# Kernel optimization log

Measured on AMD Instinct MI355X. Metric: run time of the kernel, lower is better.

The kernel has to match this reference:

```python
import jax, jax.numpy as jnp
from jax import lax
import numpy as np

TEMPERATURE = 0.8
TOP_P = 0.9
NEG_INF = -jnp.inf


def setup_inputs() -> dict:
    key = jax.random.key(0)
    k1, k2 = jax.random.split(key)
    B, V = 128, 128000
    logits = jax.random.normal(k1, (B, V), dtype=jnp.float32) * 4.0
    u = jax.random.uniform(k2, (B, 1), dtype=jnp.float32)  # replaces torch.rand in sample_multinomial
    return {"logits": logits, "u": u, "top_k": 50}


def _filtered_probs(logits, top_k):
    # temperature scaling
    x = logits / TEMPERATURE
    # ---- top-k filter: keep only the k largest per row (mask rest to -inf) ----
    kth = lax.top_k(x, top_k)[0][..., -1:]            # [B, 1] k-th largest value
    x = jnp.where(x < kth, NEG_INF, x)
    # ---- top-p (nucleus) filter ----
    sort_idx = jnp.argsort(-x, axis=-1)               # descending order, [B, V]
    sorted_x = jnp.take_along_axis(x, sort_idx, axis=-1)
    probs_sorted = jax.nn.softmax(sorted_x, axis=-1)  # -inf entries -> 0
    cdf = jnp.cumsum(probs_sorted, axis=-1)
    # remove tokens where cdf (shifted right by one, first kept) exceeds p
    remove_sorted = jnp.concatenate(
        [jnp.zeros_like(cdf[..., :1], dtype=bool), (cdf > TOP_P)[..., :-1]], axis=-1
    )
    inv = jnp.argsort(sort_idx, axis=-1)              # inverse permutation
    remove = jnp.take_along_axis(remove_sorted, inv, axis=-1)
    x = jnp.where(remove, NEG_INF, x)
    # final probabilities
    return jax.nn.softmax(x.astype(jnp.float32), axis=-1)


def reference(logits, u, top_k):
    probs = _filtered_probs(logits, top_k)            # [B, V]
    # inverse-CDF multinomial sample (matches sample_multinomial)
    csum = jnp.cumsum(probs, axis=-1)
    next_ids = jnp.sum(csum <= u, axis=-1, keepdims=True).astype(jnp.int32)  # [B, 1]
    return next_ids
```

## Files before the change

kernel.cpp:

```cpp
#include <hip/hip_runtime.h>
#include <math.h>


#define SLICES   16
#define SEGCAP   64
#define MSORT    1024

__device__ __forceinline__ unsigned fkey(float y) {
    unsigned b = __float_as_uint(y);
    return (b & 0x80000000u) ? ~b : (b | 0x80000000u);
}

__device__ __forceinline__ float block_sum(float v, int tid, float* wpart) {
#pragma unroll
    for (int off = 32; off > 0; off >>= 1) v += __shfl_down(v, off, 64);
    if ((tid & 63) == 0) wpart[tid >> 6] = v;
    __syncthreads();
    if (tid < 64) {
        float s = (tid < 16) ? wpart[tid] : 0.0f;
#pragma unroll
        for (int off = 8; off > 0; off >>= 1) s += __shfl_down(s, off, 64);
        if (tid == 0) wpart[0] = s;
    }
    __syncthreads();
    float s = wpart[0];
    __syncthreads();
    return s;
}

__device__ __forceinline__ void incl_scan(float* arr, int n, int tid, float* wpart) {
    float v = (tid < n) ? arr[tid] : 0.0f;
#pragma unroll
    for (int off = 1; off < 64; off <<= 1) {
        float o = __shfl_up(v, off, 64);
        if ((tid & 63) >= off) v += o;
    }
    if ((tid & 63) == 63) wpart[tid >> 6] = v;
    __syncthreads();
    if (tid < 64) {
        float w = (tid < 16) ? wpart[tid] : 0.0f;
#pragma unroll
        for (int off = 1; off < 16; off <<= 1) {
            float o = __shfl_up(w, off, 64);
            if (tid >= off) w += o;
        }
        if (tid < 16) wpart[tid] = w;
    }
    __syncthreads();
    const int wv = tid >> 6;
    const float base = (wv > 0) ? wpart[wv - 1] : 0.0f;
    if (tid < n) arr[tid] = v + base;
    __syncthreads();
}

__global__ __launch_bounds__(256)
void scan_kernel(const float* __restrict__ logits, int V,
                 int* __restrict__ scnt,
                 float* __restrict__ cy, int* __restrict__ ci)
{
    constexpr float YTH = 11.2f;
    __shared__ float lcy[SEGCAP];
    __shared__ int   lci[SEGCAP];
    __shared__ int   lcnt;

    const int tid = threadIdx.x;
    const int row = blockIdx.x / SLICES;
    const int sl  = blockIdx.x % SLICES;
    if (tid == 0) lcnt = 0;
    __syncthreads();

    const float* rowp = logits + (size_t)row * (size_t)V;
    const float4* rp4 = (const float4*)rowp;
    const int n4   = V >> 2;
    const int base = sl * 256 + tid;

#define PUSH4(vv, i4)                                                            \
    {                                                                            \
        float _m = fmaxf(fmaxf((vv).x, (vv).y), fmaxf((vv).z, (vv).w));          \
        if (_m >= YTH) {                                                         \
            if ((vv).x >= YTH) { int _p = atomicAdd(&lcnt, 1);                   \
                if (_p < SEGCAP) { lcy[_p] = (vv).x; lci[_p] = (i4) * 4;     } } \
            if ((vv).y >= YTH) { int _p = atomicAdd(&lcnt, 1);                   \
                if (_p < SEGCAP) { lcy[_p] = (vv).y; lci[_p] = (i4) * 4 + 1; } } \
            if ((vv).z >= YTH) { int _p = atomicAdd(&lcnt, 1);                   \
                if (_p < SEGCAP) { lcy[_p] = (vv).z; lci[_p] = (i4) * 4 + 2; } } \
            if ((vv).w >= YTH) { int _p = atomicAdd(&lcnt, 1);                   \
                if (_p < SEGCAP) { lcy[_p] = (vv).w; lci[_p] = (i4) * 4 + 3; } } \
        }                                                                        \
    }

    if (sl * 256 + 255 + 7 * 4096 < n4) {
        float4 a0 = rp4[base];
        float4 a1 = rp4[base + 4096];
        float4 a2 = rp4[base + 8192];
        float4 a3 = rp4[base + 12288];
        float4 a4 = rp4[base + 16384];
        float4 a5 = rp4[base + 20480];
        float4 a6 = rp4[base + 24576];
        float4 a7 = rp4[base + 28672];
        PUSH4(a0, base);
        PUSH4(a1, base + 4096);
        PUSH4(a2, base + 8192);
        PUSH4(a3, base + 12288);
        PUSH4(a4, base + 16384);
        PUSH4(a5, base + 20480);
        PUSH4(a6, base + 24576);
        PUSH4(a7, base + 28672);
    } else {
        const int nc = n4 - 1;
        int i0 = base,          c0 = min(i0, nc);
        int i1 = base + 4096,   c1 = min(i1, nc);
        int i2 = base + 8192,   c2 = min(i2, nc);
        int i3 = base + 12288,  c3 = min(i3, nc);
        int i4_ = base + 16384, c4 = min(i4_, nc);
        int i5 = base + 20480,  c5 = min(i5, nc);
        int i6 = base + 24576,  c6 = min(i6, nc);
        int i7 = base + 28672,  c7 = min(i7, nc);
        float4 a0 = rp4[c0];
        float4 a1 = rp4[c1];
        float4 a2 = rp4[c2];
        float4 a3 = rp4[c3];
        float4 a4 = rp4[c4];
        float4 a5 = rp4[c5];
        float4 a6 = rp4[c6];
        float4 a7 = rp4[c7];
        if (i0 < n4) PUSH4(a0, i0);
        if (i1 < n4) PUSH4(a1, i1);
        if (i2 < n4) PUSH4(a2, i2);
        if (i3 < n4) PUSH4(a3, i3);
        if (i4_ < n4) PUSH4(a4, i4_);
        if (i5 < n4) PUSH4(a5, i5);
        if (i6 < n4) PUSH4(a6, i6);
        if (i7 < n4) PUSH4(a7, i7);
    }
    for (int i = SLICES * 256 * 8 + sl * 256 + tid; i < n4; i += SLICES * 256) {
        float4 a = rp4[i];
        PUSH4(a, i);
    }
    if (sl == SLICES - 1) {
        for (int i = (n4 << 2) + tid; i < V; i += 256) {
            float y = rowp[i];
            if (y >= YTH) {
                int p = atomicAdd(&lcnt, 1);
                if (p < SEGCAP) { lcy[p] = y; lci[p] = i; }
            }
        }
    }
#undef PUSH4
    __syncthreads();

    const int cnt = lcnt;
    float* cyr = cy + ((size_t)row * SLICES + sl) * SEGCAP;
    int*   cir = ci + ((size_t)row * SLICES + sl) * SEGCAP;
    for (int p = tid; p < min(cnt, SEGCAP); p += 256) {
        cyr[p] = lcy[p];
        cir[p] = lci[p];
    }
    if (tid == 0) scnt[row * SLICES + sl] = cnt;
}

__global__ __launch_bounds__(1024)
void select_kernel(const float* __restrict__ logits,
                   const float* __restrict__ uvec,
                   const int* __restrict__ topk_p,
                   const int* __restrict__ scnt,
                   const float* __restrict__ cy, const int* __restrict__ ci,
                   int* __restrict__ out, int V)
{
    constexpr float TEMP = 0.8f;
    constexpr float TOPP = 0.9f;
    constexpr float XTH2 = 16.0f;

    __shared__ float gv[MSORT];
    __shared__ int   gi[MSORT];
    __shared__ float cv[MSORT];
    __shared__ int   cidx[MSORT];
    __shared__ float sq[MSORT];
    __shared__ float wpart[16];
    __shared__ float kth_sh;
    __shared__ int   segoff[SLICES + 1];
    __shared__ int   bad_sh, hi_cnt, cpos, scount, cnt_sh, M_sh, tie_cnt, L_cnt, ans_sh;

    const int tid  = threadIdx.x;
    const int lane = tid & 63;
    const int row  = blockIdx.x;
    const int nth  = blockDim.x;
    const int k_in = *topk_p;

    const float* rowp = logits + (size_t)row * (size_t)V;

    if (tid == 0) { hi_cnt = 0; cpos = 0; scount = 0;
                    tie_cnt = 0; L_cnt = 0; ans_sh = V; }
    if (tid < 64) {
        int c = (tid < SLICES) ? scnt[row * SLICES + tid] : 0;
        int bad = (tid < SLICES) && (c > SEGCAP);
        int acc = min(c, SEGCAP);
#pragma unroll
        for (int off = 1; off < SLICES; off <<= 1) {
            int o = __shfl_up(acc, off, 64);
            if (tid >= off) acc += o;
        }
        if (tid < SLICES) segoff[tid + 1] = acc;
        if (tid == 0) segoff[0] = 0;
        unsigned long long bm = __ballot(bad);
        if (tid == 0) bad_sh = (bm != 0ULL);
    }
    __syncthreads();

    const int M_all = segoff[SLICES];
    int M;
    if (!bad_sh && M_all >= k_in && M_all <= MSORT) {
        {
            const int s = tid >> 6;
            const int off = segoff[s];
            const int c   = segoff[s + 1] - off;
            if (lane < c) {
                const size_t base = ((size_t)row * SLICES + s) * SEGCAP + lane;
                gv[off + lane] = cy[base] / TEMP;
                gi[off + lane] = ci[base];
            }
        }
        __syncthreads();
        {
            bool pred = (tid < M_all) && (gv[tid] >= XTH2);
            unsigned long long bm = __ballot(pred);
            if (lane == 0 && bm) atomicAdd(&hi_cnt, (int)__popcll(bm));
        }
        __syncthreads();
        const float thr = (hi_cnt >= k_in) ? XTH2 : -1e38f;
        {
            bool pred = (tid < M_all) && (gv[tid] >= thr);
            unsigned long long bm = __ballot(pred);
            if (bm) {
                int fl = (int)__ffsll(bm) - 1;
                int bs = 0;
                if (pred && lane == fl) bs = atomicAdd(&cpos, (int)__popcll(bm));
                bs = __shfl(bs, fl, 64);
                if (pred) {
                    int p = bs + (int)__popcll(bm & ((1ULL << lane) - 1ULL));
                    cv[p] = gv[tid]; cidx[p] = gi[tid];
                }
            }
        }
        __syncthreads();
        M = cpos;
    } else {
        unsigned lo = 0;
        for (int bit = 31; bit >= 0; --bit) {
            unsigned t = lo | (1u << bit);
            int local = 0;
            for (int i = tid; i < V; i += nth) local += (fkey(rowp[i]) >= t);
            if (tid == 0) cnt_sh = 0;
            __syncthreads();
            atomicAdd(&cnt_sh, local);
            __syncthreads();
            if (cnt_sh >= k_in) lo = t;
            __syncthreads();
        }
        for (int i = tid; i < V; i += nth) {
            float y = rowp[i];
            if (fkey(y) >= lo) {
                int p = atomicAdd(&scount, 1);
                if (p < MSORT) { cv[p] = y / TEMP; cidx[p] = i; }
            }
        }
        __syncthreads();
        M = min(scount, MSORT);
    }
    if (tid == 0) M_sh = M;
    __syncthreads();
    M = M_sh;

    const int Mpad = (M + 3) & ~3;
    for (int t = M + tid; t < Mpad; t += nth) { cv[t] = -1e38f; cidx[t] = 0x7fffffff; }
    __syncthreads();

    if (tid < M) {
        const float v = cv[tid]; const int ix = cidx[tid];
        int r = 0;
        for (int j = 0; j < Mpad; j += 4) {
            float v0 = cv[j],     v1 = cv[j + 1];
            float v2 = cv[j + 2], v3 = cv[j + 3];
            int   i0 = cidx[j],     i1 = cidx[j + 1];
            int   i2 = cidx[j + 2], i3 = cidx[j + 3];
            r += (v0 > v || (v0 == v && i0 < ix));
            r += (v1 > v || (v1 == v && i1 < ix));
            r += (v2 > v || (v2 == v && i2 < ix));
            r += (v3 > v || (v3 == v && i3 < ix));
        }
        gv[r] = v; gi[r] = ix;
    }
    __syncthreads();

    const int kk = (M > 0) ? min(max(k_in, 1), M) : 0;
    const float mm = (M > 0) ? gv[0] : 0.0f;
    if (tid < M) cv[tid] = expf(gv[tid] - mm);
    if (tid == 0 && M > 0) kth_sh = gv[kk - 1];
    __syncthreads();

    {
        bool f = (M > 0) && (tid >= kk) && (tid < M) && (gv[tid] == kth_sh);
        unsigned long long bm = __ballot(f);
        if (lane == 0 && bm) atomicAdd(&tie_cnt, (int)__popcll(bm));
    }
    __syncthreads();
    const int Kp = kk + tie_cnt;

    const float sum1 = block_sum((tid < Kp) ? cv[tid] : 0.0f, tid, wpart);

    if (tid < Kp) sq[tid] = cv[tid] / sum1;
    incl_scan(sq, Kp, tid, wpart);
    {
        bool f = (tid >= 1) && (tid < Kp) && (sq[tid - 1] <= TOPP);
        unsigned long long bm = __ballot(f);
        if (lane == 0 && bm) atomicAdd(&L_cnt, (int)__popcll(bm));
    }
    __syncthreads();
    const int L = (M > 0) ? (1 + L_cnt) : 0;

    const float sum2 = block_sum((tid < L) ? cv[tid] : 0.0f, tid, wpart);

    if (tid < L) {
        const int ix = gi[tid];
        int r = 0;
        for (int j = 0; j < L; ++j) r += (gi[j] < ix);
        sq[r] = cv[tid] / sum2;
        cidx[r] = ix;
    }
    __syncthreads();

    incl_scan(sq, L, tid, wpart);
    {
        const float uu = uvec[row];
        bool f = (tid < L) && (sq[tid] > uu) && (tid == 0 || sq[tid - 1] <= uu);
        if (f) ans_sh = cidx[tid];
    }
    __syncthreads();
    if (tid == 0) out[row] = ans_sh;
}

extern "C" void kernel_launch(void* const* d_in, const int* in_sizes, int n_in,
                              void* d_out, int out_size, void* d_ws, size_t ws_size,
                              hipStream_t stream) {
    const float* logits = (const float*)d_in[0];
    const float* u      = (const float*)d_in[1];
    const int*   topk   = (const int*)d_in[2];
    int*         out    = (int*)d_out;

    const int B = out_size;
    const int V = in_sizes[0] / B;

    const size_t n_scnt = (size_t)B * SLICES;
    const size_t n_seg  = (size_t)B * SLICES * SEGCAP;
    int*   scnt = (int*)d_ws;
    float* cy   = (float*)((char*)d_ws + n_scnt * 4);
    int*   ci   = (int*)((char*)d_ws + n_scnt * 4 + n_seg * 4);

    scan_kernel<<<B * SLICES, 256, 0, stream>>>(logits, V, scnt, cy, ci);
    select_kernel<<<B, 1024, 0, stream>>>(logits, u, topk, scnt, cy, ci, out, V);
}
```

Baseline: 103.8 us.

## Add single-wave fast path for top-p and sampling when kept set is small

```diff
diff --git a/kernel.cpp b/kernel.cpp
--- a/kernel.cpp
+++ b/kernel.cpp
@@ -51,6 +51,20 @@
     const float base = (wv > 0) ? wpart[wv - 1] : 0.0f;
     if (tid < n) arr[tid] = v + base;
     __syncthreads();
+}
+
+__device__ __forceinline__ float wsum(float v) {
+#pragma unroll
+    for (int off = 32; off > 0; off >>= 1) v += __shfl_xor(v, off, 64);
+    return v;
+}
+__device__ __forceinline__ float wscan(float v, int lane) {
+#pragma unroll
+    for (int off = 1; off < 64; off <<= 1) {
+        float o = __shfl_up(v, off, 64);
+        if (lane >= off) v += o;
+    }
+    return v;
 }
 
 __global__ __launch_bounds__(256)
@@ -180,6 +194,7 @@
     __shared__ float kth_sh;
     __shared__ int   segoff[SLICES + 1];
     __shared__ int   bad_sh, hi_cnt, cpos, scount, cnt_sh, M_sh, tie_cnt, L_cnt, ans_sh;
+    __shared__ int   Kp_sh, fast_sh;
 
     const int tid  = threadIdx.x;
     const int lane = tid & 63;
@@ -275,8 +290,8 @@
     for (int t = M + tid; t < Mpad; t += nth) { cv[t] = -1e38f; cidx[t] = 0x7fffffff; }
     __syncthreads();
 
-    if (tid < M) {
-        const float v = cv[tid]; const int ix = cidx[tid];
+    for (int t = tid; t < M; t += nth) {
+        const float v = cv[t]; const int ix = cidx[t];
         int r = 0;
         for (int j = 0; j < Mpad; j += 4) {
             float v0 = cv[j],     v1 = cv[j + 1];
@@ -292,6 +307,87 @@
     }
     __syncthreads();
 
+    if (tid < 64) {
+        int kk = (M > 0) ? min(max(k_in, 1), M) : 0;
+        float kth = (M > 0) ? gv[kk - 1] : 0.0f;
+        int j0 = min(kk + lane, MSORT - 1);
+        int j1 = min(kk + 64 + lane, MSORT - 1);
+        bool t0 = (M > 0) && (kk + lane < M)      && (gv[j0] == kth);
+        bool t1 = (M > 0) && (kk + 64 + lane < M) && (gv[j1] == kth);
+        int cnt = (int)__popcll(__ballot(t0)) + (int)__popcll(__ballot(t1));
+        if (lane == 0) {
+            int Kp = kk + cnt;
+            Kp_sh = Kp;
+            fast_sh = (M > 0) && (Kp <= 128);
+        }
+    }
+    __syncthreads();
+
+    if (fast_sh) {
+        if (tid < 64) {
+            const int Kp = Kp_sh;
+            const int e0 = lane, e1 = lane + 64;
+            const float mm = gv[0];
+            float se0 = (e0 < Kp) ? expf(gv[e0] - mm) : 0.0f;
+            float se1 = (e1 < Kp) ? expf(gv[e1] - mm) : 0.0f;
+
+            const float sum1 = wsum(se0 + se1);
+            float q0 = se0 / sum1, q1 = se1 / sum1;
+
+            float s0 = wscan(q0, lane);
+            float T0 = __shfl(s0, 63, 64);
+            float s1 = wscan(q1, lane) + T0;
+
+            float prev0 = __shfl_up(s0, 1, 64);
+            float prev1 = __shfl_up(s1, 1, 64);
+            if (lane == 0) prev1 = T0;
+            bool c0 = (e0 >= 1) && (e0 < Kp) && (prev0 <= TOPP);
+            bool c1 = (e1 < Kp) && (prev1 <= TOPP);
+            const int L = 1 + (int)__popcll(__ballot(c0)) + (int)__popcll(__ballot(c1));
+
+            const float sum2 = wsum(((e0 < L) ? se0 : 0.0f) + ((e1 < L) ? se1 : 0.0f));
+            float p0 = se0 / sum2, p1 = se1 / sum2;
+            int i0 = (e0 < L) ? gi[e0] : 0x7fffffff;
+            int i1 = (e1 < L) ? gi[e1] : 0x7fffffff;
+
+            const int Lpad = (L + 3) & ~3;
+            if (lane < Lpad - L) gi[L + lane] = 0x7fffffff;
+            __builtin_amdgcn_wave_barrier();
+
+            int r0 = 0, r1 = 0;
+            for (int j = 0; j < Lpad; j += 4) {
+                int g0 = gi[j], g1 = gi[j + 1], g2 = gi[j + 2], g3 = gi[j + 3];
+                r0 += (g0 < i0) + (g1 < i0) + (g2 < i0) + (g3 < i0);
+                r1 += (g0 < i1) + (g1 < i1) + (g2 < i1) + (g3 < i1);
+            }
+            if (e0 < L) { sq[r0] = p0; cidx[r0] = i0; }
+            if (e1 < L) { sq[r1] = p1; cidx[r1] = i1; }
+            __builtin_amdgcn_wave_barrier();
+
+            float g0v = (e0 < L) ? sq[e0] : 0.0f;
+            float g1v = (e1 < L) ? sq[e1] : 0.0f;
+            int   vi0 = (e0 < L) ? cidx[e0] : 0;
+            int   vi1 = (e1 < L) ? cidx[e1] : 0;
+            float C0 = wscan(g0v, lane);
+            float TT = __shfl(C0, 63, 64);
+            float C1 = wscan(g1v, lane) + TT;
+            float pc0 = __shfl_up(C0, 1, 64);
+            float pc1 = __shfl_up(C1, 1, 64);
+            if (lane == 0) pc1 = TT;
+            const float uu = uvec[row];
+            bool f0 = (e0 < L) && (C0 > uu) && (e0 == 0 || pc0 <= uu);
+            bool f1 = (e1 < L) && (C1 > uu) && (pc1 <= uu);
+            int ans = V;
+            if (f0) ans = vi0;
+            if (f1) ans = vi1;
+#pragma unroll
+            for (int off = 32; off > 0; off >>= 1)
+                ans = min(ans, __shfl_xor(ans, off, 64));
+            if (lane == 0) out[row] = ans;
+        }
+        return;
+    }
+
     const int kk = (M > 0) ? min(max(k_in, 1), M) : 0;
     const float mm = (M > 0) ? gv[0] : 0.0f;
     if (tid < M) cv[tid] = expf(gv[tid] - mm);
```

New measurement: 102.0 us. Within noise of the previous version (-1.7%).
